# Performance work log

Hardware: AMD Instinct MI355X
Metric: run time of the kernel (lower is better)

The kernel has to match this reference:

```python
import jax, jax.numpy as jnp
import numpy as np

B, V, K, D, E, NE = 32, 512, 16, 128, 32, 8192


def setup_inputs() -> dict:
    key = jax.random.key(0)
    ks = jax.random.split(key, 12)
    s = 0.05
    return {
        "vertex_features": jax.random.normal(ks[0], (B, V, D), jnp.float32),
        "atom_adj": jax.random.randint(ks[1], (B * V * K,), 0, B * V),
        "bond_adj": jax.random.randint(ks[2], (B * V * K,), 0, B * NE),
        "h0": jax.random.normal(ks[3], (B, V, D), jnp.float32),
        "lamda": jnp.full((1,), 0.5, jnp.float32),
        "alpha": jnp.full((1,), 0.1, jnp.float32),
        "l": 1,
        "edge_initial": jax.random.normal(ks[4], (B, NE, E), jnp.float32),
        "vertex_mask": jnp.ones((B, V), jnp.float32),
        "nbs_mask": jax.random.uniform(ks[5], (B, V, K), jnp.float32),
        # label_U1: (D+E) -> D ; label_U2: 2D -> D ; feature_updating: D -> D (variant=False)
        "W1": jax.random.normal(ks[6], (D, D + E), jnp.float32) * s,
        "b1": jax.random.normal(ks[7], (D,), jnp.float32) * s,
        "W2": jax.random.normal(ks[8], (D, 2 * D), jnp.float32) * s,
        "b2": jax.random.normal(ks[9], (D,), jnp.float32) * s,
        "W3": jax.random.normal(ks[10], (D, D), jnp.float32) * s,
        "b3": jax.random.normal(ks[11], (D,), jnp.float32) * s,
    }


def reference(vertex_features, atom_adj, bond_adj, h0, lamda, alpha, l,
              edge_initial, vertex_mask, nbs_mask, W1, b1, W2, b2, W3, b3):
    b, v = vertex_mask.shape
    k = nbs_mask.shape[2]
    d = vertex_features.shape[-1]
    e = edge_initial.shape[-1]
    # gather neighbor vertex and edge features (flat index, torch.index_select semantics)
    vn = vertex_features.reshape(-1, d)[atom_adj].reshape(b, v, k, d)
    en = edge_initial.reshape(-1, e)[bond_adj].reshape(b, v, k, e)
    l_neighbor = jnp.concatenate([vn, en], axis=-1)            # [b,v,k,d+e]
    nl = jax.nn.gelu(l_neighbor @ W1.T + b1, approximate=False)  # exact GELU like torch F.gelu
    nl = jnp.sum(nl * nbs_mask[..., None], axis=-2)            # masked sum over neighbors -> [b,v,d]
    hi = jnp.concatenate([nl, vertex_features], axis=-1) @ W2.T + b2
    theta = jnp.log(lamda / l + 1.0)                           # broadcast scalar (shape [1])
    support = (1.0 - alpha) * hi + alpha * h0                  # variant=False: r == support
    out = theta * (support @ W3.T + b3) + (1.0 - theta) * support
    out = out + vertex_features                                # residual=True
    return out
```

## Files before the change

kernel.cpp:

```cpp
#include <hip/hip_runtime.h>
#include <hip/hip_bf16.h>
#include <math.h>

#define NLSTR 136
#define ASTR  168

typedef __bf16 bf16x8 __attribute__((ext_vector_type(8)));
typedef float f32x4 __attribute__((ext_vector_type(4)));
typedef float f32x16 __attribute__((ext_vector_type(16)));
typedef unsigned short ushort8v __attribute__((ext_vector_type(8)));

union FragU { ushort8v u; bf16x8 b; };

static __device__ inline unsigned short f2bf(float f){
  unsigned u = __float_as_uint(f);
  u += 0x7fffu + ((u >> 16) & 1u);
  return (unsigned short)(u >> 16);
}
static __device__ inline float bf2f(unsigned short u){
  return __uint_as_float(((unsigned)u) << 16);
}
static __device__ inline unsigned pk2(float a, float b){
  union { __hip_bfloat162 h; unsigned u; } r;
  r.h = __float22bfloat162_rn(float2{a, b});
  return r.u;
}
static __device__ inline ushort8v pkcvt8(float4 a, float4 b){
  union { unsigned u[4]; ushort8v v; } r;
  r.u[0] = pk2(a.x, a.y); r.u[1] = pk2(a.z, a.w);
  r.u[2] = pk2(b.x, b.y); r.u[3] = pk2(b.z, b.w);
  return r.v;
}

static __device__ inline float gelu_f(float x){
  float u = x * x;
  float p = fmaf(u, 0.07135481283f, 1.5957691216f);
  float t = x * p;
  float e = __builtin_amdgcn_exp2f(t * -1.44269504f);
  return x * __builtin_amdgcn_rcpf(1.0f + e);
}

__global__ __launch_bounds__(256) void prep_kernel(
    const float* __restrict__ vf, const float* __restrict__ W1,
    const float* __restrict__ W2, const float* __restrict__ W3,
    unsigned short* __restrict__ vfbf, unsigned short* __restrict__ w1f,
    unsigned short* __restrict__ w2f, unsigned short* __restrict__ w3f)
{
  int t = blockIdx.x * 256 + threadIdx.x;
  if (t < 262144){
    const float4* src = (const float4*)vf;
    float4 x = src[t * 2], y = src[t * 2 + 1];
    *(ushort8v*)(vfbf + t * 8) = pkcvt8(x, y);
    return;
  }
  int t2 = t - 262144;
  const float* s;
  unsigned short* d;
  if (t2 < 2560){
    int fragid = t2 >> 6, lane = t2 & 63;
    int nc2 = fragid / 10, kc = fragid % 10, n = lane & 31, h = lane >> 5;
    s = W1 + (nc2 * 32 + n) * 160 + kc * 16 + h * 8;
    d = w1f + t2 * 8;
  } else if (t2 < 6656){
    int t3 = t2 - 2560;
    int fragid = t3 >> 6, lane = t3 & 63;
    int kc = fragid >> 3, nc = fragid & 7, col = lane & 15, quad = lane >> 4;
    s = W2 + (nc * 16 + col) * 256 + kc * 32 + quad * 8;
    d = w2f + t3 * 8;
  } else if (t2 < 8704){
    int t3 = t2 - 6656;
    int fragid = t3 >> 6, lane = t3 & 63;
    int kc = fragid >> 3, nc = fragid & 7, col = lane & 15, quad = lane >> 4;
    s = W3 + (nc * 16 + col) * 128 + kc * 32 + quad * 8;
    d = w3f + t3 * 8;
  } else return;
#pragma unroll
  for (int j = 0; j < 8; j++) d[j] = f2bf(s[j]);
}

__global__ __launch_bounds__(256) void fused_kernel(
    const unsigned short* __restrict__ vfbf,
    const int* __restrict__ aadj, const int* __restrict__ badj,
    const float* __restrict__ edge, const float* __restrict__ nbs,
    const float* __restrict__ h0,
    const unsigned short* __restrict__ w1f, const unsigned short* __restrict__ w2f,
    const unsigned short* __restrict__ w3f,
    const float* __restrict__ b1, const float* __restrict__ b2, const float* __restrict__ b3,
    const float* __restrict__ lamda, const float* __restrict__ alpha,
    const int* __restrict__ lval,
    float* __restrict__ out)
{
  __shared__ __align__(16) unsigned short abuf[2][32 * ASTR];
  __shared__ __align__(16) unsigned short nl_lds[16 * NLSTR];
  __shared__ __align__(16) unsigned short sup_lds[16 * NLSTR];
  const int wid  = threadIdx.x >> 6;
  const int lane = threadIdx.x & 63;
  const int n32  = lane & 31;
  const int h    = lane >> 5;
  const int col  = lane & 15;
  const int quad = lane >> 4;
  const int v0   = blockIdx.x * 16;

  const int srow = threadIdx.x >> 3;
  const int ssub = threadIdx.x & 7;

  int a_all[8], e_all[8];
  {
    const int base = (v0 + (srow >> 4)) * 16 + (srow & 15);
#pragma unroll
    for (int p = 0; p < 8; p++){
      a_all[p] = aadj[base + 32 * p];
      e_all[p] = badj[base + 32 * p];
    }
  }

  FragU bw[10];
#pragma unroll
  for (int kc = 0; kc < 10; kc++)
    bw[kc].u = *(const ushort8v*)(w1f + ((wid * 10 + kc) * 64 + lane) * 8);

  const float bb1 = b1[wid * 32 + n32];
  const float4* nbs4 = (const float4*)nbs;

  ushort8v sv0, sv1; float4 se;
  {
    const ushort8v* vs = (const ushort8v*)(vfbf + (size_t)a_all[0] * 128 + ssub * 16);
    sv0 = vs[0]; sv1 = vs[1];
    se = *(const float4*)(edge + (size_t)e_all[0] * 32 + ssub * 4);
  }
  {
    unsigned short* dst = abuf[0] + srow * ASTR + ssub * 16;
    *(ushort8v*)dst = sv0; *(ushort8v*)(dst + 8) = sv1;
    unsigned* ed = (unsigned*)(abuf[0] + srow * ASTR + 128 + ssub * 4);
    ed[0] = pk2(se.x, se.y); ed[1] = pk2(se.z, se.w);
  }
  {
    const ushort8v* vs = (const ushort8v*)(vfbf + (size_t)a_all[1] * 128 + ssub * 16);
    sv0 = vs[0]; sv1 = vs[1];
    se = *(const float4*)(edge + (size_t)e_all[1] * 32 + ssub * 4);
  }

#pragma unroll 1
  for (int p = 0; p < 8; ++p){
    __syncthreads();

    if (p < 7){
      unsigned short* dst = abuf[(p + 1) & 1] + srow * ASTR + ssub * 16;
      *(ushort8v*)dst = sv0; *(ushort8v*)(dst + 8) = sv1;
      unsigned* ed = (unsigned*)(abuf[(p + 1) & 1] + srow * ASTR + 128 + ssub * 4);
      ed[0] = pk2(se.x, se.y); ed[1] = pk2(se.z, se.w);
    }
    if (p < 6){
      const ushort8v* vs = (const ushort8v*)(vfbf + (size_t)a_all[p + 2] * 128 + ssub * 16);
      sv0 = vs[0]; sv1 = vs[1];
      se = *(const float4*)(edge + (size_t)e_all[p + 2] * 32 + ssub * 4);
    }

    const unsigned short* ab = abuf[p & 1] + n32 * ASTR + h * 8;
    f32x16 acc = {};
#pragma unroll
    for (int kc = 0; kc < 10; kc++){
      FragU fa;
      fa.u = *(const ushort8v*)(ab + kc * 16);
      acc = __builtin_amdgcn_mfma_f32_32x32x16_bf16(fa.b, bw[kc].b, acc, 0, 0, 0);
    }

    {
      const int vA = v0 + 2 * p;
      const float4 mAlo = nbs4[vA * 4 + h],       mAhi = nbs4[vA * 4 + 2 + h];
      const float4 mBlo = nbs4[(vA + 1) * 4 + h], mBhi = nbs4[(vA + 1) * 4 + 2 + h];
      float sA = gelu_f(acc[0] + bb1) * mAlo.x + gelu_f(acc[1] + bb1) * mAlo.y
               + gelu_f(acc[2] + bb1) * mAlo.z + gelu_f(acc[3] + bb1) * mAlo.w
               + gelu_f(acc[4] + bb1) * mAhi.x + gelu_f(acc[5] + bb1) * mAhi.y
               + gelu_f(acc[6] + bb1) * mAhi.z + gelu_f(acc[7] + bb1) * mAhi.w;
      float sB = gelu_f(acc[8] + bb1) * mBlo.x + gelu_f(acc[9] + bb1) * mBlo.y
               + gelu_f(acc[10] + bb1) * mBlo.z + gelu_f(acc[11] + bb1) * mBlo.w
               + gelu_f(acc[12] + bb1) * mBhi.x + gelu_f(acc[13] + bb1) * mBhi.y
               + gelu_f(acc[14] + bb1) * mBhi.z + gelu_f(acc[15] + bb1) * mBhi.w;
      sA += __shfl_xor(sA, 32, 64);
      sB += __shfl_xor(sB, 32, 64);
      if (h == 0) nl_lds[(2 * p)     * NLSTR + wid * 32 + n32] = f2bf(sA);
      else        nl_lds[(2 * p + 1) * NLSTR + wid * 32 + n32] = f2bf(sB);
    }
  }
  __syncthreads();

  const int nc0 = 2 * wid;
  const float th = logf(lamda[0] / (float)lval[0] + 1.0f);
  const float al = alpha[0];

  f32x4 acc2[2] = {};
#pragma unroll
  for (int kc = 0; kc < 8; kc++){
    FragU a;
    if (kc < 4) a.u = *(const ushort8v*)(nl_lds + col * NLSTR + kc * 32 + quad * 8);
    else        a.u = *(const ushort8v*)(vfbf + (size_t)(v0 + col) * 128 + (kc - 4) * 32 + quad * 8);
#pragma unroll
    for (int pq = 0; pq < 2; pq++){
      FragU bf_;
      bf_.u = *(const ushort8v*)(w2f + ((kc * 8 + nc0 + pq) * 64 + lane) * 8);
      acc2[pq] = __builtin_amdgcn_mfma_f32_16x16x32_bf16(a.b, bf_.b, acc2[pq], 0, 0, 0);
    }
  }

  float sup[2][4];
#pragma unroll
  for (int pq = 0; pq < 2; pq++){
    const int d = (nc0 + pq) * 16 + col;
    const float bb = b2[d];
#pragma unroll
    for (int r = 0; r < 4; r++){
      const int vtx = v0 + quad * 4 + r;
      float hi = acc2[pq][r] + bb;
      float s = (1.f - al) * hi + al * h0[vtx * 128 + d];
      sup[pq][r] = s;
      sup_lds[(quad * 4 + r) * NLSTR + d] = f2bf(s);
    }
  }
  __syncthreads();

  f32x4 acc3[2] = {};
#pragma unroll
  for (int kc = 0; kc < 4; kc++){
    FragU a;
    a.u = *(const ushort8v*)(sup_lds + col * NLSTR + kc * 32 + quad * 8);
#pragma unroll
    for (int pq = 0; pq < 2; pq++){
      FragU bf_;
      bf_.u = *(const ushort8v*)(w3f + ((kc * 8 + nc0 + pq) * 64 + lane) * 8);
      acc3[pq] = __builtin_amdgcn_mfma_f32_16x16x32_bf16(a.b, bf_.b, acc3[pq], 0, 0, 0);
    }
  }

#pragma unroll
  for (int pq = 0; pq < 2; pq++){
    const int d = (nc0 + pq) * 16 + col;
    const float bb = b3[d];
#pragma unroll
    for (int r = 0; r < 4; r++){
      const int vtx = v0 + quad * 4 + r;
      float res = bf2f(vfbf[(size_t)vtx * 128 + d]);
      out[vtx * 128 + d] = th * (acc3[pq][r] + bb) + (1.f - th) * sup[pq][r] + res;
    }
  }
}

extern "C" void kernel_launch(void* const* d_in, const int* in_sizes, int n_in,
                              void* d_out, int out_size, void* d_ws, size_t ws_size,
                              hipStream_t stream)
{
  const float* vfp  = (const float*)d_in[0];
  const int*   aadj = (const int*)d_in[1];
  const int*   badj = (const int*)d_in[2];
  const float* h0   = (const float*)d_in[3];
  const float* lam  = (const float*)d_in[4];
  const float* alp  = (const float*)d_in[5];
  const int*   lv   = (const int*)d_in[6];
  const float* edge = (const float*)d_in[7];
  const float* nbs  = (const float*)d_in[9];
  const float* W1   = (const float*)d_in[10];
  const float* b1   = (const float*)d_in[11];
  const float* W2   = (const float*)d_in[12];
  const float* b2   = (const float*)d_in[13];
  const float* W3   = (const float*)d_in[14];
  const float* b3   = (const float*)d_in[15];
  float* out = (float*)d_out;

  unsigned short* w1f  = (unsigned short*)d_ws;
  unsigned short* w2f  = w1f + 20480;
  unsigned short* w3f  = w2f + 32768;
  unsigned short* vfbf = w3f + 16384;

  prep_kernel<<<1058, 256, 0, stream>>>(vfp, W1, W2, W3, vfbf, w1f, w2f, w3f);
  fused_kernel<<<1024, 256, 0, stream>>>(vfbf, aadj, badj, edge, nbs, h0,
                                         w1f, w2f, w3f, b1, b2, b3, lam, alp, lv, out);
}
```

Before: 142.3 us.

## Stage neighbor mask in LDS, split MFMA chains, prefetch h0 and residual

Loads the block's neighbor-mask slice into shared memory once instead of re-reading it from global memory every iteration. The main loop is fully unrolled, uses a custom barrier that waits only on LDS counters, and splits the MFMA accumulation into two independent chains to shorten the dependency chain. The h0 and residual loads are hoisted ahead of the second and third GEMMs so their latency overlaps compute. The residual now comes from fp32 vertex features instead of the bf16 copy, which also improves accuracy. Risks are the custom barrier leaving global stores or loads unsynchronised, and higher register pressure from unrolling.

```diff
diff --git a/kernel.cpp b/kernel.cpp
--- a/kernel.cpp
+++ b/kernel.cpp
@@ -39,6 +39,8 @@
   float e = __builtin_amdgcn_exp2f(t * -1.44269504f);
   return x * __builtin_amdgcn_rcpf(1.0f + e);
 }
+
+#define WG_BARRIER() asm volatile("s_waitcnt lgkmcnt(0)\n\ts_barrier" ::: "memory")
 
 __global__ __launch_bounds__(256) void prep_kernel(
     const float* __restrict__ vf, const float* __restrict__ W1,
@@ -80,6 +82,7 @@
 
 __global__ __launch_bounds__(256) void fused_kernel(
     const unsigned short* __restrict__ vfbf,
+    const float* __restrict__ vf,
     const int* __restrict__ aadj, const int* __restrict__ badj,
     const float* __restrict__ edge, const float* __restrict__ nbs,
     const float* __restrict__ h0,
@@ -93,6 +96,7 @@
   __shared__ __align__(16) unsigned short abuf[2][32 * ASTR];
   __shared__ __align__(16) unsigned short nl_lds[16 * NLSTR];
   __shared__ __align__(16) unsigned short sup_lds[16 * NLSTR];
+  __shared__ __align__(16) float nbs_lds[256];
   const int wid  = threadIdx.x >> 6;
   const int lane = threadIdx.x & 63;
   const int n32  = lane & 31;
@@ -104,6 +108,8 @@
   const int srow = threadIdx.x >> 3;
   const int ssub = threadIdx.x & 7;
 
+  nbs_lds[threadIdx.x] = nbs[v0 * 16 + threadIdx.x];
+
   int a_all[8], e_all[8];
   {
     const int base = (v0 + (srow >> 4)) * 16 + (srow & 15);
@@ -120,7 +126,6 @@
     bw[kc].u = *(const ushort8v*)(w1f + ((wid * 10 + kc) * 64 + lane) * 8);
 
   const float bb1 = b1[wid * 32 + n32];
-  const float4* nbs4 = (const float4*)nbs;
 
   ushort8v sv0, sv1; float4 se;
   {
@@ -140,9 +145,9 @@
     se = *(const float4*)(edge + (size_t)e_all[1] * 32 + ssub * 4);
   }
 
-#pragma unroll 1
+#pragma unroll
   for (int p = 0; p < 8; ++p){
-    __syncthreads();
+    WG_BARRIER();
 
     if (p < 7){
       unsigned short* dst = abuf[(p + 1) & 1] + srow * ASTR + ssub * 16;
@@ -156,19 +161,23 @@
       se = *(const float4*)(edge + (size_t)e_all[p + 2] * 32 + ssub * 4);
     }
 
+    const float4* nbsl = (const float4*)nbs_lds;
+    const float4 mAlo = nbsl[8 * p + h],     mAhi = nbsl[8 * p + 2 + h];
+    const float4 mBlo = nbsl[8 * p + 4 + h], mBhi = nbsl[8 * p + 6 + h];
+
     const unsigned short* ab = abuf[p & 1] + n32 * ASTR + h * 8;
-    f32x16 acc = {};
-#pragma unroll
-    for (int kc = 0; kc < 10; kc++){
-      FragU fa;
-      fa.u = *(const ushort8v*)(ab + kc * 16);
-      acc = __builtin_amdgcn_mfma_f32_32x32x16_bf16(fa.b, bw[kc].b, acc, 0, 0, 0);
-    }
+    f32x16 accA = {}, accB = {};
+#pragma unroll
+    for (int kc = 0; kc < 10; kc += 2){
+      FragU fa0, fa1;
+      fa0.u = *(const ushort8v*)(ab + kc * 16);
+      fa1.u = *(const ushort8v*)(ab + (kc + 1) * 16);
+      accA = __builtin_amdgcn_mfma_f32_32x32x16_bf16(fa0.b, bw[kc].b,     accA, 0, 0, 0);
+      accB = __builtin_amdgcn_mfma_f32_32x32x16_bf16(fa1.b, bw[kc + 1].b, accB, 0, 0, 0);
+    }
+    f32x16 acc = accA + accB;
 
     {
-      const int vA = v0 + 2 * p;
-      const float4 mAlo = nbs4[vA * 4 + h],       mAhi = nbs4[vA * 4 + 2 + h];
-      const float4 mBlo = nbs4[(vA + 1) * 4 + h], mBhi = nbs4[(vA + 1) * 4 + 2 + h];
       float sA = gelu_f(acc[0] + bb1) * mAlo.x + gelu_f(acc[1] + bb1) * mAlo.y
                + gelu_f(acc[2] + bb1) * mAlo.z + gelu_f(acc[3] + bb1) * mAlo.w
                + gelu_f(acc[4] + bb1) * mAhi.x + gelu_f(acc[5] + bb1) * mAhi.y
@@ -189,6 +198,15 @@
   const float th = logf(lamda[0] / (float)lval[0] + 1.0f);
   const float al = alpha[0];
 
+  float h0v[2][4];
+#pragma unroll
+  for (int pq = 0; pq < 2; pq++){
+    const int d = (nc0 + pq) * 16 + col;
+#pragma unroll
+    for (int r = 0; r < 4; r++)
+      h0v[pq][r] = h0[(v0 + quad * 4 + r) * 128 + d];
+  }
+
   f32x4 acc2[2] = {};
 #pragma unroll
   for (int kc = 0; kc < 8; kc++){
@@ -210,14 +228,22 @@
     const float bb = b2[d];
 #pragma unroll
     for (int r = 0; r < 4; r++){
-      const int vtx = v0 + quad * 4 + r;
       float hi = acc2[pq][r] + bb;
-      float s = (1.f - al) * hi + al * h0[vtx * 128 + d];
+      float s = (1.f - al) * hi + al * h0v[pq][r];
       sup[pq][r] = s;
       sup_lds[(quad * 4 + r) * NLSTR + d] = f2bf(s);
     }
   }
   __syncthreads();
+
+  float rv[2][4];
+#pragma unroll
+  for (int pq = 0; pq < 2; pq++){
+    const int d = (nc0 + pq) * 16 + col;
+#pragma unroll
+    for (int r = 0; r < 4; r++)
+      rv[pq][r] = vf[(size_t)(v0 + quad * 4 + r) * 128 + d];
+  }
 
   f32x4 acc3[2] = {};
 #pragma unroll
@@ -239,8 +265,7 @@
 #pragma unroll
     for (int r = 0; r < 4; r++){
       const int vtx = v0 + quad * 4 + r;
-      float res = bf2f(vfbf[(size_t)vtx * 128 + d]);
-      out[vtx * 128 + d] = th * (acc3[pq][r] + bb) + (1.f - th) * sup[pq][r] + res;
+      out[vtx * 128 + d] = th * (acc3[pq][r] + bb) + (1.f - th) * sup[pq][r] + rv[pq][r];
     }
   }
 }
@@ -272,6 +297,6 @@
   unsigned short* vfbf = w3f + 16384;
 
   prep_kernel<<<1058, 256, 0, stream>>>(vfp, W1, W2, W3, vfbf, w1f, w2f, w3f);
-  fused_kernel<<<1024, 256, 0, stream>>>(vfbf, aadj, badj, edge, nbs, h0,
+  fused_kernel<<<1024, 256, 0, stream>>>(vfbf, vfp, aadj, badj, edge, nbs, h0,
                                          w1f, w2f, w3f, b1, b2, b3, lam, alp, lv, out);
 }
```

New measurement: 138.1 us. 3.0% less time.
